# Kernel tuning notes

Hardware: AMD Instinct MI355X
Metric: run time of the kernel (lower is better)

The kernel has to match this reference:

```python
import jax, jax.numpy as jnp
import numpy as np

N_NODES = 50000


def _gine(x, src, dst, edge_embed, lin_w, lin_b, nn_w, nn_b):
    # PyG GINEConv (eps=0): out = nn(x + sum_{j->i} ReLU(x_j + lin(edge_attr)))
    e = edge_embed @ lin_w + lin_b              # [E, d_in]
    msg = jax.nn.relu(x[src] + e)               # gather + fuse, [E, d_in]
    agg = jax.ops.segment_sum(msg, dst, num_segments=N_NODES)  # scatter-add, [N, d_in]
    return (x + agg) @ nn_w + nn_b              # small MLP, [N, d_out]


def setup_inputs() -> dict:
    key = jax.random.key(0)
    ks = jax.random.split(key, 20)
    E = 800000
    h = 128
    sc = lambda f_in: 1.0 / np.sqrt(f_in)
    inp = {
        "x": jax.random.normal(ks[0], (N_NODES, 1), jnp.float32),
        "edge_index": jax.random.randint(ks[1], (2, E), 0, N_NODES, jnp.int64),
        "edge_attr": jax.random.normal(ks[2], (E, 1), jnp.float32),
        "em_w": jax.random.normal(ks[3], (1, h), jnp.float32) * sc(1),
        "em_b": jnp.zeros((h,), jnp.float32),
        "l1_w": jax.random.normal(ks[4], (h, 1), jnp.float32) * sc(h),
        "l1_b": jnp.zeros((1,), jnp.float32),
        "n1_w": jax.random.normal(ks[5], (1, h), jnp.float32) * sc(1),
        "n1_b": jnp.zeros((h,), jnp.float32),
        "l2_w": jax.random.normal(ks[6], (h, h), jnp.float32) * sc(h),
        "l2_b": jnp.zeros((h,), jnp.float32),
        "n2_w": jax.random.normal(ks[7], (h, h), jnp.float32) * sc(h),
        "n2_b": jnp.zeros((h,), jnp.float32),
        "l3_w": jax.random.normal(ks[8], (h, h), jnp.float32) * sc(h),
        "l3_b": jnp.zeros((h,), jnp.float32),
        "n3_w": jax.random.normal(ks[9], (h, h), jnp.float32) * sc(h),
        "n3_b": jnp.zeros((h,), jnp.float32),
        "dec_w": jax.random.normal(ks[10], (2 * h, 1), jnp.float32) * sc(2 * h),
        "dec_b": jnp.zeros((1,), jnp.float32),
    }
    return inp


def reference(x, edge_index, edge_attr, em_w, em_b, l1_w, l1_b, n1_w, n1_b,
              l2_w, l2_b, n2_w, n2_b, l3_w, l3_b, n3_w, n3_b, dec_w, dec_b):
    src, dst = edge_index[0], edge_index[1]
    edge_embed = edge_attr @ em_w + em_b                      # [E, 128]
    hdn = _gine(x,   src, dst, edge_embed, l1_w, l1_b, n1_w, n1_b)
    hdn = _gine(hdn, src, dst, edge_embed, l2_w, l2_b, n2_w, n2_b)
    hdn = _gine(hdn, src, dst, edge_embed, l3_w, l3_b, n3_w, n3_b)
    h_cat = jnp.concatenate([hdn[src], hdn[dst]], axis=-1)    # [E, 256]
    return h_cat @ dec_w + dec_b                              # [E, 1]
```

## Files before the change

kernel.cpp:

```cpp
#include <hip/hip_runtime.h>

#define H 128
#define CAPC 3072


typedef unsigned long long ull;
using bf16x8 = __attribute__((ext_vector_type(8))) short;
using f32x4  = __attribute__((ext_vector_type(4))) float;

__device__ __forceinline__ float bf2f(unsigned short v) {
  return __uint_as_float(((unsigned)v) << 16);
}
__device__ __forceinline__ unsigned short bf16r(float v) {
  unsigned u = __float_as_uint(v);
  u = (u + 0x7FFFu + ((u >> 16) & 1u)) >> 16;
  return (unsigned short)u;
}
__device__ __forceinline__ unsigned bf16pair(float a, float b) {
  return (unsigned)bf16r(a) | ((unsigned)bf16r(b) << 16);
}
__device__ __forceinline__ int rfl(int v) {
  return __builtin_amdgcn_readfirstlane(v);
}

__global__ __launch_bounds__(256) void init_consts(
    const float* __restrict__ em_w, const float* __restrict__ em_b,
    const float* __restrict__ l1_w, const float* __restrict__ l1_b,
    const float* __restrict__ l2_w, const float* __restrict__ l2_b,
    const float* __restrict__ n1_b,
    const float* __restrict__ l3_w, const float* __restrict__ l3_b,
    const float* __restrict__ n2w, const float* __restrict__ n3w,
    const float* __restrict__ n3b, const float* __restrict__ dec_w,
    float* __restrict__ consts, int* __restrict__ cursor,
    unsigned short* __restrict__ w2t) {
  if (blockIdx.x > 0) {
    const int i = (blockIdx.x - 1) * 256 + threadIdx.x;
    if (i < H * H) {
      const int j = i >> 7, k = i & (H - 1);
      w2t[k * H + j] = bf16r(n2w[i]);
    }
    return;
  }
  const int k = threadIdx.x;
  cursor[k] = 0;
  cursor[k + 256] = 0;
  __shared__ float sa[H], sc[H];
  if (k < H) {
    float u2 = 0.f, c2 = 0.f, u3 = 0.f, c3 = 0.f, vA = 0.f, vB = 0.f;
    for (int j = 0; j < H; ++j) {
      const float ew = em_w[j], eb = em_b[j];
      u2 = fmaf(ew, l2_w[j * H + k], u2);
      c2 = fmaf(eb, l2_w[j * H + k], c2);
      u3 = fmaf(ew, l3_w[j * H + k], u3);
      c3 = fmaf(eb, l3_w[j * H + k], c3);
      vA = fmaf(n3w[k * H + j], dec_w[j], vA);
      vB = fmaf(n3w[k * H + j], dec_w[H + j], vB);
    }
    consts[2 + k]         = u2;
    consts[2 + H + k]     = c2 + l2_b[k] + n1_b[k];
    consts[2 + 2 * H + k] = u3;
    consts[2 + 3 * H + k] = c3 + l3_b[k];
    consts[514 + k]       = vA;
    consts[642 + k]       = vB;
    sa[k] = em_w[k] * l1_w[k];
    sc[k] = em_b[k] * l1_w[k];
  }
  __syncthreads();
  for (int s = 64; s > 0; s >>= 1) {
    if (k < s) { sa[k] += sa[k + s]; sc[k] += sc[k + s]; }
    __syncthreads();
  }
  if (k == 0) { consts[0] = sa[0]; consts[1] = sc[0] + l1_b[0]; }
  __syncthreads();
  if (k < H) {
    sa[k] = n3b[k] * dec_w[k];
    sc[k] = n3b[k] * dec_w[H + k];
  }
  __syncthreads();
  for (int s = 64; s > 0; s >>= 1) {
    if (k < s) { sa[k] += sa[k + s]; sc[k] += sc[k + s]; }
    __syncthreads();
  }
  if (k == 0) { consts[770] = sa[0]; consts[771] = sc[0]; }
}

__global__ __launch_bounds__(1024) void bin_scatter(
    const int* __restrict__ src, const int* __restrict__ dst,
    const float* __restrict__ ea, int* __restrict__ cursor,
    ull* __restrict__ spc, int E, int NBUCK) {
  __shared__ int lhist[512];
  __shared__ int lbase[512];
  const int tid = threadIdx.x;
  const int base = blockIdx.x * 2048 + tid * 2;
  if (tid < 512) lhist[tid] = 0;
  __syncthreads();
  int s_[2], d_[2], b_[2], r_[2];
  float a_[2];
#pragma unroll
  for (int j = 0; j < 2; ++j) {
    const int e = base + j;
    if (e < E) {
      s_[j] = src[e]; d_[j] = dst[e]; a_[j] = ea[e];
      b_[j] = d_[j] >> 7;
      r_[j] = atomicAdd(&lhist[b_[j]], 1);
    } else {
      b_[j] = -1;
    }
  }
  __syncthreads();
  if (tid < NBUCK && lhist[tid] > 0)
    lbase[tid] = atomicAdd(&cursor[tid], lhist[tid]);
  __syncthreads();
#pragma unroll
  for (int j = 0; j < 2; ++j) {
    if (b_[j] >= 0) {
      const int pl = lbase[b_[j]] + r_[j];
      if (pl < CAPC)
        spc[(size_t)b_[j] * CAPC + pl] =
            ((ull)(unsigned)(s_[j] | ((d_[j] & 127) << 16)) << 32) |
            (ull)(unsigned)__float_as_uint(a_[j]);
    }
  }
}

__global__ __launch_bounds__(1024) void fine_scatter(
    const int* __restrict__ cursor, const ull* __restrict__ spc,
    const float* __restrict__ x, const float* __restrict__ consts,
    int2* __restrict__ spf, int* __restrict__ rowstart,
    float* __restrict__ s1, int N) {
  __shared__ int lh[128];
  __shared__ int sd[128];
  __shared__ int cur[128];
  __shared__ int2 pay[CAPC];
  const int tid = threadIdx.x;
  const int b = blockIdx.x;
  const int cnt = min(cursor[b], CAPC);
  const size_t rbase = (size_t)b * CAPC;
  if (tid < 128) lh[tid] = 0;
  __syncthreads();
  for (int i = tid; i < cnt; i += 1024)
    atomicAdd(&lh[(int)((spc[rbase + i] >> 48) & 127u)], 1);
  __syncthreads();
  if (tid < 128) sd[tid] = lh[tid];
  __syncthreads();
  for (int off = 1; off < 128; off <<= 1) {
    int t = 0;
    if (tid < 128 && tid >= off) t = sd[tid - off];
    __syncthreads();
    if (tid < 128) sd[tid] += t;
    __syncthreads();
  }
  if (tid < 128) {
    const int ex = sd[tid] - lh[tid];
    cur[tid] = ex;
    rowstart[b * 129 + tid] = (int)rbase + ex;
    if (tid == 0) rowstart[b * 129 + 128] = (int)rbase + cnt;
  }
  __syncthreads();
  for (int i = tid; i < cnt; i += 1024) {
    const ull payv = spc[rbase + i];
    const int dl = (int)((payv >> 48) & 127u);
    const int pos = atomicAdd(&cur[dl], 1);
    pay[pos] = make_int2((int)((payv >> 32) & 0xFFFFu), (int)(unsigned)payv);
  }
  __syncthreads();
  for (int i = tid; i < cnt; i += 1024) spf[rbase + i] = pay[i];
  const int lane = tid & 63, w = tid >> 6;
  const float a1 = consts[0], c1 = consts[1];
  for (int i = w; i < 128; i += 16) {
    const int n = (b << 7) + i;
    if (n >= N) break;
    const int rsl = sd[i] - lh[i], ci = lh[i];
    float part = 0.f;
    for (int j = lane; j < ci; j += 64) {
      const int2 pv = pay[rsl + j];
      part += fmaxf(x[pv.x] + fmaf(a1, __int_as_float(pv.y), c1), 0.f);
    }
#pragma unroll
    for (int o = 32; o >= 1; o >>= 1) part += __shfl_xor(part, o, 64);
    if (lane == 0) s1[n] = x[n] + part;
  }
}

__global__ __launch_bounds__(1024) void layer2_fused(
    const int* __restrict__ rowstart, const int2* __restrict__ sp,
    const float* __restrict__ s1, const float* __restrict__ n1w,
    const float* __restrict__ n1b, const float* __restrict__ consts,
    const unsigned short* __restrict__ w2t, const float* __restrict__ n2b,
    unsigned short* __restrict__ h2b, int N) {
  __shared__ unsigned short t2s[16][136];
  __shared__ unsigned short hs[16][128];
  const int tid = threadIdx.x, w = tid >> 6, lane = tid & 63;
  const int node0 = blockIdx.x * 16;
  {
    const int n = rfl(node0 + w);
    if (n < N) {
      const int rb = (n >> 7) * 129 + (n & 127);
      const int rs = rfl(rowstart[rb]), re = rfl(rowstart[rb + 1]);
      const float w0 = n1w[lane],            w1 = n1w[lane + 64];
      const float u0 = consts[2 + lane],     u1 = consts[2 + lane + 64];
      const float c0 = consts[2 + H + lane], c1 = consts[2 + H + lane + 64];
      float acc0 = 0.f, acc1 = 0.f;
      int j = rs;
      for (; j + 4 <= re; j += 4) {
        int sx[4];
        float av[4], sv[4];
#pragma unroll
        for (int u = 0; u < 4; ++u) {
          const int2 ev = sp[j + u];
          sx[u] = rfl(ev.x);
          av[u] = __int_as_float(rfl(ev.y));
        }
#pragma unroll
        for (int u = 0; u < 4; ++u) sv[u] = s1[sx[u]];
#pragma unroll
        for (int u = 0; u < 4; ++u) {
          acc0 += fmaxf(fmaf(sv[u], w0, fmaf(av[u], u0, c0)), 0.f);
          acc1 += fmaxf(fmaf(sv[u], w1, fmaf(av[u], u1, c1)), 0.f);
        }
      }
      for (; j < re; ++j) {
        const int2 ev = sp[j];
        const int sx = rfl(ev.x);
        const float av = __int_as_float(rfl(ev.y));
        const float sv = s1[sx];
        acc0 += fmaxf(fmaf(sv, w0, fmaf(av, u0, c0)), 0.f);
        acc1 += fmaxf(fmaf(sv, w1, fmaf(av, u1, c1)), 0.f);
      }
      const float sn = s1[n];
      t2s[w][lane]      = bf16r(fmaf(sn, w0, n1b[lane])      + acc0);
      t2s[w][lane + 64] = bf16r(fmaf(sn, w1, n1b[lane + 64]) + acc1);
    } else {
      t2s[w][lane] = 0;
      t2s[w][lane + 64] = 0;
    }
  }
  __syncthreads();
  if (w < 8) {
    const int t = w, col = lane & 15, quad = lane >> 4;
    const bf16x8 a0 = *(const bf16x8*)&t2s[col][quad * 8];
    const bf16x8 a1 = *(const bf16x8*)&t2s[col][32 + quad * 8];
    const bf16x8 a2 = *(const bf16x8*)&t2s[col][64 + quad * 8];
    const bf16x8 a3 = *(const bf16x8*)&t2s[col][96 + quad * 8];
    const bf16x8* bcol =
        (const bf16x8*)(w2t + (size_t)(t * 16 + col) * H + quad * 8);
    f32x4 acc = {0.f, 0.f, 0.f, 0.f};
    acc = __builtin_amdgcn_mfma_f32_16x16x32_bf16(a0, bcol[0], acc, 0, 0, 0);
    acc = __builtin_amdgcn_mfma_f32_16x16x32_bf16(a1, bcol[4], acc, 0, 0, 0);
    acc = __builtin_amdgcn_mfma_f32_16x16x32_bf16(a2, bcol[8], acc, 0, 0, 0);
    acc = __builtin_amdgcn_mfma_f32_16x16x32_bf16(a3, bcol[12], acc, 0, 0, 0);
    const float bias = n2b[t * 16 + col];
#pragma unroll
    for (int r = 0; r < 4; ++r)
      hs[quad * 4 + r][t * 16 + col] = bf16r(acc[r] + bias);
  }
  __syncthreads();
  const int row = tid >> 6, word = tid & 63;
  ((unsigned*)h2b)[(size_t)(node0 + row) * 64 + word] =
      ((const unsigned*)hs)[row * 64 + word];
}

__global__ __launch_bounds__(256) void layer3_dot(
    const int* __restrict__ rowstart, const int2* __restrict__ sp,
    const unsigned short* __restrict__ h2b, const float* __restrict__ consts,
    float* __restrict__ p, float* __restrict__ q, int N) {
  const int n = rfl((blockIdx.x * blockDim.x + threadIdx.x) >> 6);
  const int lane = threadIdx.x & 63;
  if (n >= N) return;
  const int k0 = 2 * lane;
  const float u0 = consts[2 + 2 * H + k0], u1 = consts[2 + 2 * H + k0 + 1];
  const float c0 = consts[2 + 3 * H + k0], c1 = consts[2 + 3 * H + k0 + 1];
  const float vA0 = consts[514 + k0], vA1 = consts[514 + k0 + 1];
  const float vB0 = consts[642 + k0], vB1 = consts[642 + k0 + 1];
  const int rb = (n >> 7) * 129 + (n & 127);
  const int rs = rfl(rowstart[rb]), re = rfl(rowstart[rb + 1]);
  float acc0 = 0.f, acc1 = 0.f;
  int j = rs;
  for (; j + 8 <= re; j += 8) {
    int ss[8];
    float aa[8];
    ushort2 hh[8];
#pragma unroll
    for (int u = 0; u < 8; ++u) {
      const int2 ev = sp[j + u];
      ss[u] = rfl(ev.x);
      aa[u] = __int_as_float(rfl(ev.y));
    }
#pragma unroll
    for (int u = 0; u < 8; ++u)
      hh[u] = *(const ushort2*)&h2b[(size_t)ss[u] * H + k0];
#pragma unroll
    for (int u = 0; u < 8; ++u) {
      acc0 += fmaxf(bf2f(hh[u].x) + fmaf(aa[u], u0, c0), 0.f);
      acc1 += fmaxf(bf2f(hh[u].y) + fmaf(aa[u], u1, c1), 0.f);
    }
  }
  for (; j + 4 <= re; j += 4) {
    int ss[4];
    float aa[4];
    ushort2 hh[4];
#pragma unroll
    for (int u = 0; u < 4; ++u) {
      const int2 ev = sp[j + u];
      ss[u] = rfl(ev.x);
      aa[u] = __int_as_float(rfl(ev.y));
    }
#pragma unroll
    for (int u = 0; u < 4; ++u)
      hh[u] = *(const ushort2*)&h2b[(size_t)ss[u] * H + k0];
#pragma unroll
    for (int u = 0; u < 4; ++u) {
      acc0 += fmaxf(bf2f(hh[u].x) + fmaf(aa[u], u0, c0), 0.f);
      acc1 += fmaxf(bf2f(hh[u].y) + fmaf(aa[u], u1, c1), 0.f);
    }
  }
  for (; j < re; ++j) {
    const int2 ev = sp[j];
    const int s0 = rfl(ev.x);
    const float a0 = __int_as_float(rfl(ev.y));
    const ushort2 hv = *(const ushort2*)&h2b[(size_t)s0 * H + k0];
    acc0 += fmaxf(bf2f(hv.x) + fmaf(a0, u0, c0), 0.f);
    acc1 += fmaxf(bf2f(hv.y) + fmaf(a0, u1, c1), 0.f);
  }
  const ushort2 hn = *(const ushort2*)&h2b[(size_t)n * H + k0];
  const float t0 = bf2f(hn.x) + acc0;
  const float t1 = bf2f(hn.y) + acc1;
  float pd = t0 * vA0 + t1 * vA1;
  float qd = t0 * vB0 + t1 * vB1;
#pragma unroll
  for (int o = 32; o >= 1; o >>= 1) {
    pd += __shfl_xor(pd, o, 64);
    qd += __shfl_xor(qd, o, 64);
  }
  if (lane == 0) {
    p[n] = pd + consts[770];
    q[n] = qd + consts[771];
  }
}

__global__ void final_kernel(const int* __restrict__ src,
                             const int* __restrict__ dst,
                             const float* __restrict__ p,
                             const float* __restrict__ q,
                             const float* __restrict__ dec_b,
                             float* __restrict__ out, int E) {
  const int e0 = (blockIdx.x * blockDim.x + threadIdx.x) * 2;
  if (e0 + 1 < E) {
    const int2 s2 = *(const int2*)&src[e0];
    const int2 d2 = *(const int2*)&dst[e0];
    const float db = dec_b[0];
    float2 o;
    o.x = p[s2.x] + q[d2.x] + db;
    o.y = p[s2.y] + q[d2.y] + db;
    *(float2*)&out[e0] = o;
  } else if (e0 < E) {
    out[e0] = p[src[e0]] + q[dst[e0]] + dec_b[0];
  }
}

extern "C" void kernel_launch(void* const* d_in, const int* in_sizes, int n_in,
                              void* d_out, int out_size, void* d_ws, size_t ws_size,
                              hipStream_t stream) {
  const float* x     = (const float*)d_in[0];
  const int*   ei    = (const int*)d_in[1];
  const float* ea    = (const float*)d_in[2];
  const float* em_w  = (const float*)d_in[3];
  const float* em_b  = (const float*)d_in[4];
  const float* l1_w  = (const float*)d_in[5];
  const float* l1_b  = (const float*)d_in[6];
  const float* n1_w  = (const float*)d_in[7];
  const float* n1_b  = (const float*)d_in[8];
  const float* l2_w  = (const float*)d_in[9];
  const float* l2_b  = (const float*)d_in[10];
  const float* n2_w  = (const float*)d_in[11];
  const float* n2_b  = (const float*)d_in[12];
  const float* l3_w  = (const float*)d_in[13];
  const float* l3_b  = (const float*)d_in[14];
  const float* n3_w  = (const float*)d_in[15];
  const float* n3_b  = (const float*)d_in[16];
  const float* dec_w = (const float*)d_in[17];
  const float* dec_b = (const float*)d_in[18];
  float* out = (float*)d_out;

  const int N = in_sizes[0];
  const int E = in_sizes[2];
  const int* src = ei;
  const int* dst = ei + E;

  const int NBUCK  = (N + 127) >> 7;
  const int NBATCH = (E + 2047) >> 11;
  const int NPAD   = ((N + 15) / 16) * 16;
  const int NT16   = NPAD / 16;

  float* ws       = (float*)d_ws;
  float* consts   = ws;
  ull*   spc      = (ull*)(ws + 1024);
  int2*  spf      = (int2*)(spc + (size_t)NBUCK * CAPC);
  unsigned short* h2b = (unsigned short*)(spf + (size_t)NBUCK * CAPC);
  unsigned short* w2t = h2b + (size_t)NPAD * H;
  float* s1       = (float*)(w2t + H * H);
  float* p        = s1 + N;
  float* q        = p + N;
  int*   cursor   = (int*)(q + N);
  int*   rowstart = cursor + 512;

  init_consts<<<65, 256, 0, stream>>>(em_w, em_b, l1_w, l1_b, l2_w, l2_b,
                                      n1_b, l3_w, l3_b, n2_w, n3_w, n3_b,
                                      dec_w, consts, cursor, w2t);
  bin_scatter<<<NBATCH, 1024, 0, stream>>>(src, dst, ea, cursor, spc, E, NBUCK);
  fine_scatter<<<NBUCK, 1024, 0, stream>>>(cursor, spc, x, consts, spf,
                                           rowstart, s1, N);
  layer2_fused<<<NT16, 1024, 0, stream>>>(rowstart, spf, s1, n1_w, n1_b,
                                          consts, w2t, n2_b, h2b, N);
  layer3_dot<<<(N + 3) / 4, 256, 0, stream>>>(rowstart, spf, h2b, consts,
                                              p, q, N);
  final_kernel<<<(E / 2 + 255) / 256, 256, 0, stream>>>(src, dst, p, q, dec_b,
                                                        out, E);
}
```

Baseline: 213.6 us.

## Merge init and binning kernels, prefetch edge records, split accumulators in gathers

The constant-setup and weight-transpose work is folded into the edge-binning kernel, so one launch does both. The bucket cursor becomes a device global that the final kernel resets to zero for the next call, which removes the in-stream zeroing dependency. The layer-2 and layer-3 gather loops now prefetch the next batch of edge records while processing the current one, and use extra partial accumulators for more ILP. The cost is more register pressure, plus reliance on cross-call cursor state that stays correct only if every run completes.

```diff
diff --git a/kernel.cpp b/kernel.cpp
--- a/kernel.cpp
+++ b/kernel.cpp
@@ -7,6 +7,8 @@
 typedef unsigned long long ull;
 using bf16x8 = __attribute__((ext_vector_type(8))) short;
 using f32x4  = __attribute__((ext_vector_type(4))) float;
+
+__device__ int g_cursor[512];
 
 __device__ __forceinline__ float bf2f(unsigned short v) {
   return __uint_as_float(((unsigned)v) << 16);
@@ -16,14 +18,13 @@
   u = (u + 0x7FFFu + ((u >> 16) & 1u)) >> 16;
   return (unsigned short)u;
 }
-__device__ __forceinline__ unsigned bf16pair(float a, float b) {
-  return (unsigned)bf16r(a) | ((unsigned)bf16r(b) << 16);
-}
 __device__ __forceinline__ int rfl(int v) {
   return __builtin_amdgcn_readfirstlane(v);
 }
 
-__global__ __launch_bounds__(256) void init_consts(
+__global__ __launch_bounds__(1024) void init_bin(
+    const int* __restrict__ src, const int* __restrict__ dst,
+    const float* __restrict__ ea,
     const float* __restrict__ em_w, const float* __restrict__ em_b,
     const float* __restrict__ l1_w, const float* __restrict__ l1_b,
     const float* __restrict__ l2_w, const float* __restrict__ l2_b,
@@ -31,67 +32,61 @@
     const float* __restrict__ l3_w, const float* __restrict__ l3_b,
     const float* __restrict__ n2w, const float* __restrict__ n3w,
     const float* __restrict__ n3b, const float* __restrict__ dec_w,
-    float* __restrict__ consts, int* __restrict__ cursor,
-    unsigned short* __restrict__ w2t) {
-  if (blockIdx.x > 0) {
-    const int i = (blockIdx.x - 1) * 256 + threadIdx.x;
-    if (i < H * H) {
-      const int j = i >> 7, k = i & (H - 1);
-      w2t[k * H + j] = bf16r(n2w[i]);
-    }
+    float* __restrict__ consts, unsigned short* __restrict__ w2t,
+    ull* __restrict__ spc, int E, int NBUCK) {
+  const int bid = blockIdx.x;
+  const int tid = threadIdx.x;
+  if (bid == 0) {
+    __shared__ float sa[H], sc[H];
+    const int k = tid;
+    if (k < H) {
+      float u2 = 0.f, c2 = 0.f, u3 = 0.f, c3 = 0.f, vA = 0.f, vB = 0.f;
+      for (int j = 0; j < H; ++j) {
+        const float ew = em_w[j], eb = em_b[j];
+        u2 = fmaf(ew, l2_w[j * H + k], u2);
+        c2 = fmaf(eb, l2_w[j * H + k], c2);
+        u3 = fmaf(ew, l3_w[j * H + k], u3);
+        c3 = fmaf(eb, l3_w[j * H + k], c3);
+        vA = fmaf(n3w[k * H + j], dec_w[j], vA);
+        vB = fmaf(n3w[k * H + j], dec_w[H + j], vB);
+      }
+      consts[2 + k]         = u2;
+      consts[2 + H + k]     = c2 + l2_b[k] + n1_b[k];
+      consts[2 + 2 * H + k] = u3;
+      consts[2 + 3 * H + k] = c3 + l3_b[k];
+      consts[514 + k]       = vA;
+      consts[642 + k]       = vB;
+      sa[k] = em_w[k] * l1_w[k];
+      sc[k] = em_b[k] * l1_w[k];
+    }
+    __syncthreads();
+    for (int s = 64; s > 0; s >>= 1) {
+      if (k < s) { sa[k] += sa[k + s]; sc[k] += sc[k + s]; }
+      __syncthreads();
+    }
+    if (k == 0) { consts[0] = sa[0]; consts[1] = sc[0] + l1_b[0]; }
+    __syncthreads();
+    if (k < H) {
+      sa[k] = n3b[k] * dec_w[k];
+      sc[k] = n3b[k] * dec_w[H + k];
+    }
+    __syncthreads();
+    for (int s = 64; s > 0; s >>= 1) {
+      if (k < s) { sa[k] += sa[k + s]; sc[k] += sc[k + s]; }
+      __syncthreads();
+    }
+    if (k == 0) { consts[770] = sa[0]; consts[771] = sc[0]; }
     return;
   }
-  const int k = threadIdx.x;
-  cursor[k] = 0;
-  cursor[k + 256] = 0;
-  __shared__ float sa[H], sc[H];
-  if (k < H) {
-    float u2 = 0.f, c2 = 0.f, u3 = 0.f, c3 = 0.f, vA = 0.f, vB = 0.f;
-    for (int j = 0; j < H; ++j) {
-      const float ew = em_w[j], eb = em_b[j];
-      u2 = fmaf(ew, l2_w[j * H + k], u2);
-      c2 = fmaf(eb, l2_w[j * H + k], c2);
-      u3 = fmaf(ew, l3_w[j * H + k], u3);
-      c3 = fmaf(eb, l3_w[j * H + k], c3);
-      vA = fmaf(n3w[k * H + j], dec_w[j], vA);
-      vB = fmaf(n3w[k * H + j], dec_w[H + j], vB);
-    }
-    consts[2 + k]         = u2;
-    consts[2 + H + k]     = c2 + l2_b[k] + n1_b[k];
-    consts[2 + 2 * H + k] = u3;
-    consts[2 + 3 * H + k] = c3 + l3_b[k];
-    consts[514 + k]       = vA;
-    consts[642 + k]       = vB;
-    sa[k] = em_w[k] * l1_w[k];
-    sc[k] = em_b[k] * l1_w[k];
-  }
-  __syncthreads();
-  for (int s = 64; s > 0; s >>= 1) {
-    if (k < s) { sa[k] += sa[k + s]; sc[k] += sc[k + s]; }
-    __syncthreads();
-  }
-  if (k == 0) { consts[0] = sa[0]; consts[1] = sc[0] + l1_b[0]; }
-  __syncthreads();
-  if (k < H) {
-    sa[k] = n3b[k] * dec_w[k];
-    sc[k] = n3b[k] * dec_w[H + k];
-  }
-  __syncthreads();
-  for (int s = 64; s > 0; s >>= 1) {
-    if (k < s) { sa[k] += sa[k + s]; sc[k] += sc[k + s]; }
-    __syncthreads();
-  }
-  if (k == 0) { consts[770] = sa[0]; consts[771] = sc[0]; }
-}
-
-__global__ __launch_bounds__(1024) void bin_scatter(
-    const int* __restrict__ src, const int* __restrict__ dst,
-    const float* __restrict__ ea, int* __restrict__ cursor,
-    ull* __restrict__ spc, int E, int NBUCK) {
+  if (bid <= 16) {
+    const int i = (bid - 1) * 1024 + tid;
+    const int j = i >> 7, k = i & (H - 1);
+    w2t[k * H + j] = bf16r(n2w[i]);
+    return;
+  }
   __shared__ int lhist[512];
   __shared__ int lbase[512];
-  const int tid = threadIdx.x;
-  const int base = blockIdx.x * 2048 + tid * 2;
+  const int base = (bid - 17) * 2048 + tid * 2;
   if (tid < 512) lhist[tid] = 0;
   __syncthreads();
   int s_[2], d_[2], b_[2], r_[2];
@@ -109,7 +104,7 @@
   }
   __syncthreads();
   if (tid < NBUCK && lhist[tid] > 0)
-    lbase[tid] = atomicAdd(&cursor[tid], lhist[tid]);
+    lbase[tid] = atomicAdd(&g_cursor[tid], lhist[tid]);
   __syncthreads();
 #pragma unroll
   for (int j = 0; j < 2; ++j) {
@@ -124,17 +119,16 @@
 }
 
 __global__ __launch_bounds__(1024) void fine_scatter(
-    const int* __restrict__ cursor, const ull* __restrict__ spc,
-    const float* __restrict__ x, const float* __restrict__ consts,
-    int2* __restrict__ spf, int* __restrict__ rowstart,
-    float* __restrict__ s1, int N) {
+    const ull* __restrict__ spc, const float* __restrict__ x,
+    const float* __restrict__ consts, int2* __restrict__ spf,
+    int* __restrict__ rowstart, float* __restrict__ s1, int N) {
   __shared__ int lh[128];
   __shared__ int sd[128];
   __shared__ int cur[128];
   __shared__ int2 pay[CAPC];
   const int tid = threadIdx.x;
   const int b = blockIdx.x;
-  const int cnt = min(cursor[b], CAPC);
+  const int cnt = min(g_cursor[b], CAPC);
   const size_t rbase = (size_t)b * CAPC;
   if (tid < 128) lh[tid] = 0;
   __syncthreads();
@@ -197,36 +191,49 @@
     if (n < N) {
       const int rb = (n >> 7) * 129 + (n & 127);
       const int rs = rfl(rowstart[rb]), re = rfl(rowstart[rb + 1]);
-      const float w0 = n1w[lane],            w1 = n1w[lane + 64];
-      const float u0 = consts[2 + lane],     u1 = consts[2 + lane + 64];
-      const float c0 = consts[2 + H + lane], c1 = consts[2 + H + lane + 64];
-      float acc0 = 0.f, acc1 = 0.f;
+      const float w0 = n1w[lane],             w1 = n1w[lane + 64];
+      const float u0 = consts[2 + lane],      u1 = consts[2 + lane + 64];
+      const float cc0 = consts[2 + H + lane], cc1 = consts[2 + H + lane + 64];
+      float acc0 = 0.f, acc1 = 0.f, acc2 = 0.f, acc3 = 0.f;
+      auto proc4 = [&](const int2 e0, const int2 e1, const int2 e2,
+                       const int2 e3) {
+        const int x0 = rfl(e0.x), x1 = rfl(e1.x), x2 = rfl(e2.x),
+                  x3 = rfl(e3.x);
+        const float a0 = __int_as_float(rfl(e0.y));
+        const float a1 = __int_as_float(rfl(e1.y));
+        const float a2 = __int_as_float(rfl(e2.y));
+        const float a3 = __int_as_float(rfl(e3.y));
+        const float v0 = s1[x0], v1 = s1[x1], v2 = s1[x2], v3 = s1[x3];
+        acc0 += fmaxf(fmaf(v0, w0, fmaf(a0, u0, cc0)), 0.f);
+        acc1 += fmaxf(fmaf(v0, w1, fmaf(a0, u1, cc1)), 0.f);
+        acc2 += fmaxf(fmaf(v1, w0, fmaf(a1, u0, cc0)), 0.f);
+        acc3 += fmaxf(fmaf(v1, w1, fmaf(a1, u1, cc1)), 0.f);
+        acc0 += fmaxf(fmaf(v2, w0, fmaf(a2, u0, cc0)), 0.f);
+        acc1 += fmaxf(fmaf(v2, w1, fmaf(a2, u1, cc1)), 0.f);
+        acc2 += fmaxf(fmaf(v3, w0, fmaf(a3, u0, cc0)), 0.f);
+        acc3 += fmaxf(fmaf(v3, w1, fmaf(a3, u1, cc1)), 0.f);
+      };
       int j = rs;
-      for (; j + 4 <= re; j += 4) {
-        int sx[4];
-        float av[4], sv[4];
-#pragma unroll
-        for (int u = 0; u < 4; ++u) {
-          const int2 ev = sp[j + u];
-          sx[u] = rfl(ev.x);
-          av[u] = __int_as_float(rfl(ev.y));
+      if (re - rs >= 4) {
+        int2 e0 = sp[j], e1 = sp[j + 1], e2 = sp[j + 2], e3 = sp[j + 3];
+        for (j += 4; j + 4 <= re; j += 4) {
+          const int2 t0 = sp[j], t1 = sp[j + 1], t2 = sp[j + 2],
+                     t3 = sp[j + 3];
+          proc4(e0, e1, e2, e3);
+          e0 = t0; e1 = t1; e2 = t2; e3 = t3;
         }
-#pragma unroll
-        for (int u = 0; u < 4; ++u) sv[u] = s1[sx[u]];
-#pragma unroll
-        for (int u = 0; u < 4; ++u) {
-          acc0 += fmaxf(fmaf(sv[u], w0, fmaf(av[u], u0, c0)), 0.f);
-          acc1 += fmaxf(fmaf(sv[u], w1, fmaf(av[u], u1, c1)), 0.f);
-        }
+        proc4(e0, e1, e2, e3);
       }
       for (; j < re; ++j) {
         const int2 ev = sp[j];
         const int sx = rfl(ev.x);
         const float av = __int_as_float(rfl(ev.y));
         const float sv = s1[sx];
-        acc0 += fmaxf(fmaf(sv, w0, fmaf(av, u0, c0)), 0.f);
-        acc1 += fmaxf(fmaf(sv, w1, fmaf(av, u1, c1)), 0.f);
+        acc0 += fmaxf(fmaf(sv, w0, fmaf(av, u0, cc0)), 0.f);
+        acc1 += fmaxf(fmaf(sv, w1, fmaf(av, u1, cc1)), 0.f);
       }
+      acc0 += acc2;
+      acc1 += acc3;
       const float sn = s1[n];
       t2s[w][lane]      = bf16r(fmaf(sn, w0, n1b[lane])      + acc0);
       t2s[w][lane + 64] = bf16r(fmaf(sn, w1, n1b[lane + 64]) + acc1);
@@ -274,28 +281,46 @@
   const float vB0 = consts[642 + k0], vB1 = consts[642 + k0 + 1];
   const int rb = (n >> 7) * 129 + (n & 127);
   const int rs = rfl(rowstart[rb]), re = rfl(rowstart[rb + 1]);
-  float acc0 = 0.f, acc1 = 0.f;
-  int j = rs;
-  for (; j + 8 <= re; j += 8) {
+  float acc0 = 0.f, acc1 = 0.f, acc2 = 0.f, acc3 = 0.f;
+  auto proc8 = [&](const int2* cb) {
     int ss[8];
     float aa[8];
     ushort2 hh[8];
 #pragma unroll
     for (int u = 0; u < 8; ++u) {
-      const int2 ev = sp[j + u];
-      ss[u] = rfl(ev.x);
-      aa[u] = __int_as_float(rfl(ev.y));
+      ss[u] = rfl(cb[u].x);
+      aa[u] = __int_as_float(rfl(cb[u].y));
     }
 #pragma unroll
     for (int u = 0; u < 8; ++u)
       hh[u] = *(const ushort2*)&h2b[(size_t)ss[u] * H + k0];
 #pragma unroll
     for (int u = 0; u < 8; ++u) {
-      acc0 += fmaxf(bf2f(hh[u].x) + fmaf(aa[u], u0, c0), 0.f);
-      acc1 += fmaxf(bf2f(hh[u].y) + fmaf(aa[u], u1, c1), 0.f);
-    }
-  }
-  for (; j + 4 <= re; j += 4) {
+      if (u & 1) {
+        acc2 += fmaxf(bf2f(hh[u].x) + fmaf(aa[u], u0, c0), 0.f);
+        acc3 += fmaxf(bf2f(hh[u].y) + fmaf(aa[u], u1, c1), 0.f);
+      } else {
+        acc0 += fmaxf(bf2f(hh[u].x) + fmaf(aa[u], u0, c0), 0.f);
+        acc1 += fmaxf(bf2f(hh[u].y) + fmaf(aa[u], u1, c1), 0.f);
+      }
+    }
+  };
+  int j = rs;
+  if (re - rs >= 8) {
+    int2 cb[8];
+#pragma unroll
+    for (int u = 0; u < 8; ++u) cb[u] = sp[j + u];
+    for (j += 8; j + 8 <= re; j += 8) {
+      int2 tb[8];
+#pragma unroll
+      for (int u = 0; u < 8; ++u) tb[u] = sp[j + u];
+      proc8(cb);
+#pragma unroll
+      for (int u = 0; u < 8; ++u) cb[u] = tb[u];
+    }
+    proc8(cb);
+  }
+  if (j + 4 <= re) {
     int ss[4];
     float aa[4];
     ushort2 hh[4];
@@ -313,6 +338,7 @@
       acc0 += fmaxf(bf2f(hh[u].x) + fmaf(aa[u], u0, c0), 0.f);
       acc1 += fmaxf(bf2f(hh[u].y) + fmaf(aa[u], u1, c1), 0.f);
     }
+    j += 4;
   }
   for (; j < re; ++j) {
     const int2 ev = sp[j];
@@ -322,6 +348,8 @@
     acc0 += fmaxf(bf2f(hv.x) + fmaf(a0, u0, c0), 0.f);
     acc1 += fmaxf(bf2f(hv.y) + fmaf(a0, u1, c1), 0.f);
   }
+  acc0 += acc2;
+  acc1 += acc3;
   const ushort2 hn = *(const ushort2*)&h2b[(size_t)n * H + k0];
   const float t0 = bf2f(hn.x) + acc0;
   const float t1 = bf2f(hn.y) + acc1;
@@ -344,6 +372,10 @@
                              const float* __restrict__ q,
                              const float* __restrict__ dec_b,
                              float* __restrict__ out, int E) {
+  if (blockIdx.x == 0 && threadIdx.x < 256) {
+    g_cursor[threadIdx.x] = 0;
+    g_cursor[threadIdx.x + 256] = 0;
+  }
   const int e0 = (blockIdx.x * blockDim.x + threadIdx.x) * 2;
   if (e0 + 1 < E) {
     const int2 s2 = *(const int2*)&src[e0];
@@ -401,15 +433,13 @@
   float* s1       = (float*)(w2t + H * H);
   float* p        = s1 + N;
   float* q        = p + N;
-  int*   cursor   = (int*)(q + N);
-  int*   rowstart = cursor + 512;
-
-  init_consts<<<65, 256, 0, stream>>>(em_w, em_b, l1_w, l1_b, l2_w, l2_b,
-                                      n1_b, l3_w, l3_b, n2_w, n3_w, n3_b,
-                                      dec_w, consts, cursor, w2t);
-  bin_scatter<<<NBATCH, 1024, 0, stream>>>(src, dst, ea, cursor, spc, E, NBUCK);
-  fine_scatter<<<NBUCK, 1024, 0, stream>>>(cursor, spc, x, consts, spf,
-                                           rowstart, s1, N);
+  int*   rowstart = (int*)(q + N) + 512;
+
+  init_bin<<<17 + NBATCH, 1024, 0, stream>>>(
+      src, dst, ea, em_w, em_b, l1_w, l1_b, l2_w, l2_b, n1_b, l3_w, l3_b,
+      n2_w, n3_w, n3_b, dec_w, consts, w2t, spc, E, NBUCK);
+  fine_scatter<<<NBUCK, 1024, 0, stream>>>(spc, x, consts, spf, rowstart,
+                                           s1, N);
   layer2_fused<<<NT16, 1024, 0, stream>>>(rowstart, spf, s1, n1_w, n1_b,
                                           consts, w2t, n2_b, h2b, N);
   layer3_dot<<<(N + 3) / 4, 256, 0, stream>>>(rowstart, spf, h2b, consts,
```

Result: faster. 208.0 us (-2.6%).
